# Performance work log

Measured on AMD Instinct MI355X. Metric: run time of the kernel, lower is better.

## Reference

```python
import jax, jax.numpy as jnp
import numpy as np

B, T, V = 64, 512, 32


def setup_inputs() -> dict:
    key = jax.random.key(0)
    k0, k1, k2, k3, k4, k5 = jax.random.split(key, 6)
    scores = jax.random.normal(k0, (B, T, V, V), dtype=jnp.float32)
    targets = jax.random.randint(k1, (B, T + 1), 0, V, dtype=jnp.int64)
    w_tx = jax.random.normal(k2, (V, V), dtype=jnp.float32) * 0.1
    w_init = jax.random.normal(k3, (V,), dtype=jnp.float32) * 0.1
    w_final = jax.random.normal(k4, (V,), dtype=jnp.float32) * 0.1
    w_dur = jax.random.normal(k5, (V, V), dtype=jnp.float32) * 0.1
    return {"scores": scores, "targets": targets, "w_tx": w_tx,
            "w_init": w_init, "w_final": w_final, "w_dur": w_dur}


def reference(scores, targets, w_tx, w_init, w_final, w_dur):
    """LatticeCrf.log_prob: per-sequence log p(y | x).

    Path score for states s_0..s_T:
      w_init[s_0] + w_final[s_T] + sum_t (scores[t, s_{t-1}, s_t] + w_tx + w_dur).
    Denominator is the CRF partition function via a forward scan over the
    [V,V] transition lattice (equivalent to obs o duration o transition FST
    composition followed by forward_score in the gtn original, with the
    default duration length D=1).
    """
    Bn, Tn, Vn, _ = scores.shape
    # per-frame combined arc weights: obs + transition + duration  [B,T,V,V]
    step = scores + (w_tx + w_dur)[None, None]

    def body(alpha, st):  # alpha [B,V], st [B,V,V]
        new = jax.nn.logsumexp(alpha[:, :, None] + st, axis=1)
        return new, None

    alpha0 = jnp.broadcast_to(w_init[None, :], (Bn, Vn))
    alphaT, _ = jax.lax.scan(body, alpha0, jnp.moveaxis(step, 1, 0))
    log_denom = jax.nn.logsumexp(alphaT + w_final[None, :], axis=-1)  # [B]

    src, dst = targets[:, :-1], targets[:, 1:]  # [B,T]
    b = jnp.arange(Bn)[:, None]
    t = jnp.arange(Tn)[None, :]
    log_num = (step[b, t, src, dst].sum(-1)
               + w_init[targets[:, 0]] + w_final[targets[:, -1]])  # [B]
    return log_num - log_denom
```

## Files before the change

### kernel.cpp

```cpp
#include <hip/hip_runtime.h>

#define BB 64
#define TT 512
#define VV 32
#define LOG2E 1.4426950408889634f
#define LN2f  0.6931471805599453f
#define SHIFT 6.0f

typedef __bf16 bf16x8 __attribute__((ext_vector_type(8)));
typedef float  f32x16 __attribute__((ext_vector_type(16)));

union Frag { unsigned int u[4]; bf16x8 v; };

__device__ __forceinline__ unsigned int pack_bf16(float lo, float hi) {
    unsigned int a = __float_as_uint(lo) + 0x8000u;
    unsigned int b = __float_as_uint(hi) + 0x8000u;
    return __builtin_amdgcn_perm(b, a, 0x07060302u);
}

__global__ __launch_bounds__(256) void crf_chunk_kernel(
    const float* __restrict__ scores,
    const float* __restrict__ w_tx,
    const float* __restrict__ w_dur,
    float* __restrict__ ws_M,
    int CC, int L)
{
    const int lane = threadIdx.x & 63;
    const int wid  = threadIdx.x >> 6;
    const int chunk = blockIdx.x * 4 + wid;
    const int m = lane & 31;
    const int h = lane >> 5;

    const int base = h * 128 + m;

    float w2[16];
#pragma unroll
    for (int j = 0; j < 8; ++j) {
        const int off = base + (j & 3) * 32 + (j >> 2) * 256;
        w2[j]     = (w_tx[off]       + w_dur[off])       * LOG2E - SHIFT;
        w2[j + 8] = (w_tx[off + 512] + w_dur[off + 512]) * LOG2E - SHIFT;
    }

    const int b = chunk / CC, c = chunk - b * CC;
    const float* sc = scores + ((size_t)(b * TT + c * L)) * 1024 + base;

    float s[16];
#pragma unroll
    for (int j = 0; j < 8; ++j) {
        const int off = (j & 3) * 32 + (j >> 2) * 256;
        s[j]     = sc[off];
        s[j + 8] = sc[off + 512];
    }

    f32x16 acc;
#pragma unroll
    for (int r = 0; r < 16; ++r) {
        const int mr = (r & 3) + 8 * (r >> 2) + 4 * h;
        acc[r] = (mr == m) ? 1.0f : 0.0f;
    }

    for (int t = 0; t < L; ++t) {
        float fa[16];
#pragma unroll
        for (int j = 0; j < 16; ++j) fa[j] = __builtin_fmaf(s[j], LOG2E, w2[j]);

        if (t + 1 < L) {
            const float* sn = sc + (size_t)(t + 1) * 1024;
#pragma unroll
            for (int j = 0; j < 8; ++j) {
                const int off = (j & 3) * 32 + (j >> 2) * 256;
                s[j]     = sn[off];
                s[j + 8] = sn[off + 512];
            }
        }

        float e[16];
#pragma unroll
        for (int j = 0; j < 16; ++j) e[j] = __builtin_amdgcn_exp2f(fa[j]);

        Frag a1, a2, b1, b2;
#pragma unroll
        for (int p = 0; p < 4; ++p) {
            a1.u[p] = pack_bf16(e[2 * p],        e[2 * p + 1]);
            a2.u[p] = pack_bf16(e[8 + 2 * p],    e[8 + 2 * p + 1]);
            b1.u[p] = pack_bf16(acc[2 * p],      acc[2 * p + 1]);
            b2.u[p] = pack_bf16(acc[8 + 2 * p],  acc[8 + 2 * p + 1]);
        }

        f32x16 z;
#pragma unroll
        for (int r = 0; r < 16; ++r) z[r] = 0.0f;
        f32x16 tmp = __builtin_amdgcn_mfma_f32_32x32x16_bf16(a1.v, b1.v, z,   0, 0, 0);
        acc        = __builtin_amdgcn_mfma_f32_32x32x16_bf16(a2.v, b2.v, tmp, 0, 0, 0);
    }

    float* outP = ws_M + (size_t)chunk * 1024;
#pragma unroll
    for (int r = 0; r < 16; ++r) {
        const int mr = (r & 3) + 8 * (r >> 2) + 4 * h;
        outP[mr * 32 + m] = acc[r];
    }
}

__global__ __launch_bounds__(64) void crf_combine_kernel(
    const float* __restrict__ scores,
    const int*   __restrict__ targets,
    const float* __restrict__ w_tx,
    const float* __restrict__ w_init,
    const float* __restrict__ w_final,
    const float* __restrict__ w_dur,
    const float* __restrict__ ws_M,
    float* __restrict__ out,
    int CC)
{
    const int b    = blockIdx.x;
    const int lane = threadIdx.x;

    const int* tg = targets + b * (TT + 1);
    float num = 0.f;
#pragma unroll
    for (int k = 0; k < TT / 64; ++k) {
        const int t  = lane + 64 * k;
        const int s_ = tg[t];
        const int d_ = tg[t + 1];
        const int wi = s_ * VV + d_;
        num += scores[(((size_t)b * TT + t) * VV + s_) * VV + d_] + w_tx[wi] + w_dur[wi];
    }
#pragma unroll
    for (int mS = 32; mS >= 1; mS >>= 1) num += __shfl_xor(num, mS, 64);

    const int j = lane & 31;
    float a    = __builtin_amdgcn_exp2f(w_init[j] * LOG2E);
    float accl = 0.f;
    const float* Pb = ws_M + (size_t)b * CC * 1024;

    float4 rr[8];
#pragma unroll
    for (int q = 0; q < 8; ++q) rr[q] = *(const float4*)(Pb + j * 32 + 4 * q);

    for (int c = 0; c < CC; ++c) {
        float4 rn[8];
        if (c + 1 < CC) {
            const float* Pn = Pb + (size_t)(c + 1) * 1024 + j * 32;
#pragma unroll
            for (int q = 0; q < 8; ++q) rn[q] = *(const float4*)(Pn + 4 * q);
        }
        float an = 0.f;
#pragma unroll
        for (int i = 0; i < 32; ++i) {
            const float  ai = __shfl(a, i, 32);
            const float4 v  = rr[i >> 2];
            const float  pv = ((i & 3) == 0) ? v.x : ((i & 3) == 1) ? v.y
                             : ((i & 3) == 2) ? v.z : v.w;
            an = __builtin_fmaf(ai, pv, an);
        }
        float mx = an;
#pragma unroll
        for (int mS = 16; mS >= 1; mS >>= 1) mx = fmaxf(mx, __shfl_xor(mx, mS, 32));
        a = an / mx;
        accl += __builtin_amdgcn_logf(mx);
        if (c + 1 < CC) {
#pragma unroll
            for (int q = 0; q < 8; ++q) rr[q] = rn[q];
        }
    }

    float rf = a * __builtin_amdgcn_exp2f(w_final[j] * LOG2E);
    float ss = rf;
#pragma unroll
    for (int mS = 16; mS >= 1; mS >>= 1) ss += __shfl_xor(ss, mS, 32);
    const float denom_ln =
        (__builtin_amdgcn_logf(ss) + accl + SHIFT * (float)TT) * LN2f;

    if (lane == 0) {
        out[b] = num + w_init[tg[0]] + w_final[tg[TT]] - denom_ln;
    }
}

extern "C" void kernel_launch(void* const* d_in, const int* in_sizes, int n_in,
                              void* d_out, int out_size, void* d_ws, size_t ws_size,
                              hipStream_t stream) {
    const float* scores  = (const float*)d_in[0];
    const int*   targets = (const int*)d_in[1];
    const float* w_tx    = (const float*)d_in[2];
    const float* w_init  = (const float*)d_in[3];
    const float* w_final = (const float*)d_in[4];
    const float* w_dur   = (const float*)d_in[5];
    float*       out     = (float*)d_out;
    float*       ws_M    = (float*)d_ws;

    int CC = 8;
    if      (ws_size >= (size_t)BB * 32 * 4096) CC = 32;
    else if (ws_size >= (size_t)BB * 16 * 4096) CC = 16;
    const int L = TT / CC;

    crf_chunk_kernel<<<BB * CC / 4, 256, 0, stream>>>(scores, w_tx, w_dur, ws_M, CC, L);
    crf_combine_kernel<<<BB, 64, 0, stream>>>(scores, targets, w_tx, w_init,
                                              w_final, w_dur, ws_M, out, CC);
}
```

Measured before the change: 234.6 us.

## Template chunk kernel on length, double-buffer score prefetch, allow more chunks

Makes the chunk length a template parameter so the time loop fully unrolls, and prefetches scores two steps ahead with a double buffer to hide global load latency behind the exp and MFMA chain. It also adds a 64-chunk configuration when the workspace is large enough, which raises parallelism in the chunk kernel but lengthens the serial combine loop. The 16-chunk option is dropped, so mid-size workspaces now fall back to 8 chunks. Unrolling raises register pressure.

```diff
diff --git a/kernel.cpp b/kernel.cpp
--- a/kernel.cpp
+++ b/kernel.cpp
@@ -18,15 +18,16 @@
     return __builtin_amdgcn_perm(b, a, 0x07060302u);
 }
 
+template <int L>
 __global__ __launch_bounds__(256) void crf_chunk_kernel(
     const float* __restrict__ scores,
     const float* __restrict__ w_tx,
     const float* __restrict__ w_dur,
-    float* __restrict__ ws_M,
-    int CC, int L)
+    float* __restrict__ ws_M)
 {
-    const int lane = threadIdx.x & 63;
-    const int wid  = threadIdx.x >> 6;
+    constexpr int CC = TT / L;
+    const int lane  = threadIdx.x & 63;
+    const int wid   = threadIdx.x >> 6;
     const int chunk = blockIdx.x * 4 + wid;
     const int m = lane & 31;
     const int h = lane >> 5;
@@ -44,12 +45,20 @@
     const int b = chunk / CC, c = chunk - b * CC;
     const float* sc = scores + ((size_t)(b * TT + c * L)) * 1024 + base;
 
-    float s[16];
+    float s[2][16];
 #pragma unroll
     for (int j = 0; j < 8; ++j) {
         const int off = (j & 3) * 32 + (j >> 2) * 256;
-        s[j]     = sc[off];
-        s[j + 8] = sc[off + 512];
+        s[0][j]     = sc[off];
+        s[0][j + 8] = sc[off + 512];
+    }
+    if (L > 1) {
+#pragma unroll
+        for (int j = 0; j < 8; ++j) {
+            const int off = 1024 + (j & 3) * 32 + (j >> 2) * 256;
+            s[1][j]     = sc[off];
+            s[1][j + 8] = sc[off + 512];
+        }
     }
 
     f32x16 acc;
@@ -59,37 +68,38 @@
         acc[r] = (mr == m) ? 1.0f : 0.0f;
     }
 
+    f32x16 z;
+#pragma unroll
+    for (int r = 0; r < 16; ++r) z[r] = 0.0f;
+
+#pragma unroll
     for (int t = 0; t < L; ++t) {
-        float fa[16];
-#pragma unroll
-        for (int j = 0; j < 16; ++j) fa[j] = __builtin_fmaf(s[j], LOG2E, w2[j]);
-
-        if (t + 1 < L) {
-            const float* sn = sc + (size_t)(t + 1) * 1024;
+        const int bk = t & 1;
+
+        float e[16];
+#pragma unroll
+        for (int j = 0; j < 16; ++j)
+            e[j] = __builtin_amdgcn_exp2f(__builtin_fmaf(s[bk][j], LOG2E, w2[j]));
+
+        if (t + 2 < L) {
+            const float* sn = sc + (size_t)(t + 2) * 1024;
 #pragma unroll
             for (int j = 0; j < 8; ++j) {
                 const int off = (j & 3) * 32 + (j >> 2) * 256;
-                s[j]     = sn[off];
-                s[j + 8] = sn[off + 512];
+                s[bk][j]     = sn[off];
+                s[bk][j + 8] = sn[off + 512];
             }
         }
 
-        float e[16];
-#pragma unroll
-        for (int j = 0; j < 16; ++j) e[j] = __builtin_amdgcn_exp2f(fa[j]);
-
         Frag a1, a2, b1, b2;
 #pragma unroll
         for (int p = 0; p < 4; ++p) {
-            a1.u[p] = pack_bf16(e[2 * p],        e[2 * p + 1]);
-            a2.u[p] = pack_bf16(e[8 + 2 * p],    e[8 + 2 * p + 1]);
-            b1.u[p] = pack_bf16(acc[2 * p],      acc[2 * p + 1]);
-            b2.u[p] = pack_bf16(acc[8 + 2 * p],  acc[8 + 2 * p + 1]);
-        }
-
-        f32x16 z;
-#pragma unroll
-        for (int r = 0; r < 16; ++r) z[r] = 0.0f;
+            a1.u[p] = pack_bf16(e[2 * p],       e[2 * p + 1]);
+            a2.u[p] = pack_bf16(e[8 + 2 * p],   e[8 + 2 * p + 1]);
+            b1.u[p] = pack_bf16(acc[2 * p],     acc[2 * p + 1]);
+            b2.u[p] = pack_bf16(acc[8 + 2 * p], acc[8 + 2 * p + 1]);
+        }
+
         f32x16 tmp = __builtin_amdgcn_mfma_f32_32x32x16_bf16(a1.v, b1.v, z,   0, 0, 0);
         acc        = __builtin_amdgcn_mfma_f32_32x32x16_bf16(a2.v, b2.v, tmp, 0, 0, 0);
     }
@@ -189,12 +199,17 @@
     float*       out     = (float*)d_out;
     float*       ws_M    = (float*)d_ws;
 
-    int CC = 8;
-    if      (ws_size >= (size_t)BB * 32 * 4096) CC = 32;
-    else if (ws_size >= (size_t)BB * 16 * 4096) CC = 16;
-    const int L = TT / CC;
-
-    crf_chunk_kernel<<<BB * CC / 4, 256, 0, stream>>>(scores, w_tx, w_dur, ws_M, CC, L);
+    int CC;
+    if (ws_size >= (size_t)BB * 64 * 4096) {
+        CC = 64;
+        crf_chunk_kernel<8><<<BB * CC / 4, 256, 0, stream>>>(scores, w_tx, w_dur, ws_M);
+    } else if (ws_size >= (size_t)BB * 32 * 4096) {
+        CC = 32;
+        crf_chunk_kernel<16><<<BB * CC / 4, 256, 0, stream>>>(scores, w_tx, w_dur, ws_M);
+    } else {
+        CC = 8;
+        crf_chunk_kernel<64><<<BB * CC / 4, 256, 0, stream>>>(scores, w_tx, w_dur, ws_M);
+    }
     crf_combine_kernel<<<BB, 64, 0, stream>>>(scores, targets, w_tx, w_init,
                                               w_final, w_dur, ws_M, out, CC);
 }
```

Result: slower. 263.3 us (+12.2%).
